# Kernel optimization log

Hardware: AMD Instinct MI355X
Metric: run time of the kernel (lower is better)

The kernel has to match this reference:

```python
import jax, jax.numpy as jnp
import numpy as np

EMBED_DIM = 768
NUM_HEADS = 12
HEAD_DIM = EMBED_DIM // NUM_HEADS
MLP_HIDDEN = int(EMBED_DIM * 4.0)
LN_EPS = 1e-5


def setup_inputs() -> dict:
    key = jax.random.key(0)
    ks = jax.random.split(key, 8)
    C, H = EMBED_DIM, MLP_HIDDEN
    s = 0.02
    return {
        "x": jax.random.normal(ks[0], (2, 2048, C), dtype=jnp.float32),
        "ln1_g": jnp.ones((C,), jnp.float32),
        "ln1_b": jnp.zeros((C,), jnp.float32),
        "qkv_w": jax.random.normal(ks[1], (3 * C, C), jnp.float32) * s,
        "proj_w": jax.random.normal(ks[2], (C, C), jnp.float32) * s,
        "proj_b": jnp.zeros((C,), jnp.float32),
        "ln2_g": jnp.ones((C,), jnp.float32),
        "ln2_b": jnp.zeros((C,), jnp.float32),
        "fc1_w": jax.random.normal(ks[3], (H, C), jnp.float32) * s,
        "fc1_b": jnp.zeros((H,), jnp.float32),
        "fc2_w": jax.random.normal(ks[4], (C, H), jnp.float32) * s,
        "fc2_b": jnp.zeros((C,), jnp.float32),
    }


def _layernorm(x, g, b):
    mu = jnp.mean(x, axis=-1, keepdims=True)
    var = jnp.mean(jnp.square(x - mu), axis=-1, keepdims=True)
    return (x - mu) * jax.lax.rsqrt(var + LN_EPS) * g + b


def reference(x, ln1_g, ln1_b, qkv_w, proj_w, proj_b, ln2_g, ln2_b,
              fc1_w, fc1_b, fc2_w, fc2_b):
    B, N, C = x.shape
    Hh, Dh = NUM_HEADS, HEAD_DIM
    scale = Dh ** -0.5

    # --- attention branch (pre-norm) ---
    h = _layernorm(x, ln1_g, ln1_b)
    qkv = h @ qkv_w.T                                   # [B,N,3C]
    qkv = qkv.reshape(B, N, 3, Hh, Dh)
    q = qkv[:, :, 0].transpose(0, 2, 1, 3)              # [B,H,N,D]
    k = qkv[:, :, 1].transpose(0, 2, 1, 3)
    v = qkv[:, :, 2].transpose(0, 2, 1, 3)
    attn = jnp.einsum('bhnd,bhmd->bhnm', q, k) * scale  # [B,H,N,N]
    attn = jax.nn.softmax(attn, axis=-1)
    o = jnp.einsum('bhnm,bhmd->bhnd', attn, v)          # [B,H,N,D]
    o = o.transpose(0, 2, 1, 3).reshape(B, N, C)
    x = x + o @ proj_w.T + proj_b

    # --- MLP branch (pre-norm), exact GELU like nn.GELU ---
    h = _layernorm(x, ln2_g, ln2_b)
    h = jax.nn.gelu(h @ fc1_w.T + fc1_b, approximate=False)
    x = x + h @ fc2_w.T + fc2_b
    return x
```

## Files before the change

kernel.cpp:

```cpp
#include <hip/hip_runtime.h>
#include <hip/hip_bf16.h>
#include <cstdint>
#include <math.h>


typedef __bf16 bf16_t;
typedef bf16_t bf16x4 __attribute__((ext_vector_type(4)));
typedef bf16_t bf16x8 __attribute__((ext_vector_type(8)));
typedef float floatx4 __attribute__((ext_vector_type(4)));

#define AS1 __attribute__((address_space(1)))
#define AS3 __attribute__((address_space(3)))

__device__ __forceinline__ void async_load16(const void* g, void* l) {
  const AS1 unsigned int* gp =
      reinterpret_cast<const AS1 unsigned int*>(reinterpret_cast<uintptr_t>(g));
  AS3 unsigned int* lp = reinterpret_cast<AS3 unsigned int*>(
      static_cast<unsigned int>(reinterpret_cast<uintptr_t>(l)));
  __builtin_amdgcn_global_load_lds(gp, lp, 16, 0, 0);
}

__device__ __forceinline__ bf16x8 lds_read8(const bf16_t* p) {
  return *reinterpret_cast<const bf16x8*>(p);
}

__global__ __launch_bounds__(256) void cvt_k(const float* __restrict__ in,
                                             bf16_t* __restrict__ out, int n4) {
  const int i = blockIdx.x * 256 + threadIdx.x;
  if (i < n4) {
    const float4 v = reinterpret_cast<const float4*>(in)[i];
    bf16x4 o;
    o[0] = (bf16_t)v.x; o[1] = (bf16_t)v.y; o[2] = (bf16_t)v.z; o[3] = (bf16_t)v.w;
    reinterpret_cast<bf16x4*>(out)[i] = o;
  }
}

__global__ __launch_bounds__(256) void ln_k(const float* __restrict__ x,
                                            const float* __restrict__ g,
                                            const float* __restrict__ b,
                                            bf16_t* __restrict__ out) {
  const int row = blockIdx.x;
  const int tid = threadIdx.x;
  const float* xr = x + (long)row * 768;
  float v[3];
#pragma unroll
  for (int e = 0; e < 3; e++) v[e] = xr[tid + e * 256];
  float s = v[0] + v[1] + v[2];
  float ss = v[0] * v[0] + v[1] * v[1] + v[2] * v[2];
#pragma unroll
  for (int off = 32; off >= 1; off >>= 1) {
    s += __shfl_down(s, off, 64);
    ss += __shfl_down(ss, off, 64);
  }
  __shared__ float red[8];
  __shared__ float stat[2];
  const int wv = tid >> 6;
  if ((tid & 63) == 0) { red[wv] = s; red[4 + wv] = ss; }
  __syncthreads();
  if (tid == 0) {
    float S = red[0] + red[1] + red[2] + red[3];
    float SS = red[4] + red[5] + red[6] + red[7];
    float mu = S * (1.0f / 768.0f);
    float var = SS * (1.0f / 768.0f) - mu * mu;
    stat[0] = mu;
    stat[1] = rsqrtf(var + 1e-5f);
  }
  __syncthreads();
  const float mu = stat[0], rs = stat[1];
#pragma unroll
  for (int e = 0; e < 3; e++) {
    int c = tid + e * 256;
    out[(long)row * 768 + c] = (bf16_t)((v[e] - mu) * rs * g[c] + b[c]);
  }
}

template <int MODE>
__global__ __launch_bounds__(256, 2) void gemm_k(
    const bf16_t* __restrict__ A, const bf16_t* __restrict__ Bt, int lda,
    int ldb, int keff, int Nld, const float* __restrict__ bias,
    bf16_t* __restrict__ out_bf, bf16_t* __restrict__ q_out,
    bf16_t* __restrict__ k_out, bf16_t* __restrict__ vt_out) {
  constexpr int BK = 32;
  __shared__ __align__(16) bf16_t As[2][128 * BK];
  __shared__ __align__(16) bf16_t Bs[2][128 * BK];

  const int tid = threadIdx.x;
  const int w = tid >> 6;
  const int lane = tid & 63;
  const int quad = lane >> 4;
  const int lid = lane & 15;
  const int wr = (w >> 1) * 64;
  const int wc = (w & 1) * 64;
  const int mBase = blockIdx.y * 128;
  const int nBase = blockIdx.x * 128;

  const int ldsRowSub = lane >> 2;
  const int kblk = (lane & 3) ^ (ldsRowSub & 3);
  const int rq0 = (quad ^ (lid & 3)) * 8;
  const int c0 = w * 2, c1 = w * 2 + 1;
  const int rowA0 = c0 * 16 + ldsRowSub, rowA1 = c1 * 16 + ldsRowSub;

  const bf16_t* Ag = A + (long)mBase * lda;
  const bf16_t* Bg = Bt + (long)nBase * ldb;

  floatx4 acc[4][4];
#pragma unroll
  for (int i = 0; i < 4; i++)
#pragma unroll
    for (int j = 0; j < 4; j++) acc[i][j] = (floatx4){0.f, 0.f, 0.f, 0.f};

  async_load16(Ag + (long)rowA0 * lda + kblk * 8, &As[0][c0 * 512]);
  async_load16(Ag + (long)rowA1 * lda + kblk * 8, &As[0][c1 * 512]);
  async_load16(Bg + (long)rowA0 * ldb + kblk * 8, &Bs[0][c0 * 512]);
  async_load16(Bg + (long)rowA1 * ldb + kblk * 8, &Bs[0][c1 * 512]);

  const int iters = keff / BK;
  int cur = 0;
  for (int it = 0; it < iters; it++) {
    __syncthreads();
    if (it + 1 < iters) {
      const int k0 = (it + 1) * BK;
      const int nb = cur ^ 1;
      async_load16(Ag + (long)rowA0 * lda + k0 + kblk * 8, &As[nb][c0 * 512]);
      async_load16(Ag + (long)rowA1 * lda + k0 + kblk * 8, &As[nb][c1 * 512]);
      async_load16(Bg + (long)rowA0 * ldb + k0 + kblk * 8, &Bs[nb][c0 * 512]);
      async_load16(Bg + (long)rowA1 * ldb + k0 + kblk * 8, &Bs[nb][c1 * 512]);
    }

    bf16x8 af[4], bfv[4];
#pragma unroll
    for (int i = 0; i < 4; i++)
      af[i] = lds_read8(&As[cur][(wr + i * 16 + lid) * BK + rq0]);
#pragma unroll
    for (int j = 0; j < 4; j++)
      bfv[j] = lds_read8(&Bs[cur][(wc + j * 16 + lid) * BK + rq0]);
#pragma unroll
    for (int i = 0; i < 4; i++)
#pragma unroll
      for (int j = 0; j < 4; j++)
        acc[i][j] = __builtin_amdgcn_mfma_f32_16x16x32_bf16(af[i], bfv[j],
                                                            acc[i][j], 0, 0, 0);
    cur ^= 1;
  }

#pragma unroll
  for (int i = 0; i < 4; i++) {
    const int mRow = mBase + wr + i * 16 + quad * 4;
#pragma unroll
    for (int j = 0; j < 4; j++) {
      const int n = nBase + wc + j * 16 + lid;
      if constexpr (MODE == 0) {
        const int which = n / 768;
        const int rem = n - which * 768;
        const int head = rem >> 6;
        const int d = rem & 63;
        const int b = mRow >> 11;
        const int t = mRow & 2047;
        const int bh = b * 12 + head;
        if (which == 2) {
          bf16x4 pk;
#pragma unroll
          for (int r = 0; r < 4; r++) pk[r] = (bf16_t)acc[i][j][r];
          const long off = ((long)bh * 64 + d) * 2048 + t;
          *reinterpret_cast<bf16x4*>(&vt_out[off]) = pk;
        } else if (which == 0) {
#pragma unroll
          for (int r = 0; r < 4; r++)
            q_out[((long)bh * 2048 + t + r) * 64 + d] =
                (bf16_t)(acc[i][j][r] * 0.125f);
        } else {
#pragma unroll
          for (int r = 0; r < 4; r++)
            k_out[((long)bh * 2048 + t + r) * 64 + d] = (bf16_t)acc[i][j][r];
        }
      } else {
        const float bv = bias[n];
#pragma unroll
        for (int r = 0; r < 4; r++) {
          float v = acc[i][j][r] + bv;
          float ge = 0.5f * v * (1.0f + erff(v * 0.70710678118654752f));
          out_bf[(long)(mRow + r) * Nld + n] = (bf16_t)ge;
        }
      }
    }
  }
}

template <int MODE>
__global__ __launch_bounds__(256, 2) void gemm64_k(
    const bf16_t* __restrict__ A, const bf16_t* __restrict__ Bt, int lda,
    int ldb, int keff, int Nld, const float* __restrict__ bias,
    const float* __restrict__ resid_f, float* __restrict__ out_f) {
  constexpr int BK = 32;
  __shared__ __align__(16) bf16_t As[2][128 * BK];
  __shared__ __align__(16) bf16_t Bs[2][64 * BK];

  const int tid = threadIdx.x;
  const int w = tid >> 6;
  const int lane = tid & 63;
  const int quad = lane >> 4;
  const int lid = lane & 15;
  const int mBase = blockIdx.y * 128;
  const int nBase = blockIdx.x * 64;

  const int ldsRowSub = lane >> 2;
  const int kblk = (lane & 3) ^ (ldsRowSub & 3);
  const int rq0 = (quad ^ (lid & 3)) * 8;
  const int rowA0 = w * 16 + ldsRowSub;
  const int rowA1 = (w + 4) * 16 + ldsRowSub;

  const bf16_t* Ag = A + (long)mBase * lda;
  const bf16_t* Bg = Bt + (long)nBase * ldb;

  floatx4 acc[2][4];
#pragma unroll
  for (int i = 0; i < 2; i++)
#pragma unroll
    for (int j = 0; j < 4; j++) acc[i][j] = (floatx4){0.f, 0.f, 0.f, 0.f};

  async_load16(Ag + (long)rowA0 * lda + kblk * 8, &As[0][w * 512]);
  async_load16(Ag + (long)rowA1 * lda + kblk * 8, &As[0][(w + 4) * 512]);
  async_load16(Bg + (long)rowA0 * ldb + kblk * 8, &Bs[0][w * 512]);

  const int iters = keff / BK;
  int cur = 0;
  for (int it = 0; it < iters; it++) {
    __syncthreads();
    if (it + 1 < iters) {
      const int k0 = (it + 1) * BK;
      const int nb = cur ^ 1;
      async_load16(Ag + (long)rowA0 * lda + k0 + kblk * 8, &As[nb][w * 512]);
      async_load16(Ag + (long)rowA1 * lda + k0 + kblk * 8, &As[nb][(w + 4) * 512]);
      async_load16(Bg + (long)rowA0 * ldb + k0 + kblk * 8, &Bs[nb][w * 512]);
    }

    bf16x8 af[2], bfv[4];
#pragma unroll
    for (int i = 0; i < 2; i++)
      af[i] = lds_read8(&As[cur][(w * 32 + i * 16 + lid) * BK + rq0]);
#pragma unroll
    for (int j = 0; j < 4; j++)
      bfv[j] = lds_read8(&Bs[cur][(j * 16 + lid) * BK + rq0]);
#pragma unroll
    for (int i = 0; i < 2; i++)
#pragma unroll
      for (int j = 0; j < 4; j++)
        acc[i][j] = __builtin_amdgcn_mfma_f32_16x16x32_bf16(af[i], bfv[j],
                                                            acc[i][j], 0, 0, 0);
    cur ^= 1;
  }

#pragma unroll
  for (int i = 0; i < 2; i++) {
    const int mRow = mBase + w * 32 + i * 16 + quad * 4;
#pragma unroll
    for (int j = 0; j < 4; j++) {
      const int n = nBase + j * 16 + lid;
      if constexpr (MODE == 1) {
        const float bv = bias[n];
#pragma unroll
        for (int r = 0; r < 4; r++) {
          const long off = (long)(mRow + r) * Nld + n;
          out_f[off] = resid_f[off] + acc[i][j][r] + bv;
        }
      } else {
#pragma unroll
        for (int r = 0; r < 4; r++) {
          const long off = (long)(mRow + r) * Nld + n;
          out_f[off] += acc[i][j][r];
        }
      }
    }
  }
}

__global__ __launch_bounds__(256, 2) void flash_k(const bf16_t* __restrict__ q,
                                                  const bf16_t* __restrict__ kk,
                                                  const bf16_t* __restrict__ vt,
                                                  bf16_t* __restrict__ o) {
  constexpr int SK = 64, D = 64, PS = 68;
  __shared__ __align__(16) bf16_t Ks[2][SK * D];
  __shared__ __align__(16) bf16_t Vs[3][D * SK];
  __shared__ __align__(16) bf16_t Ps[4][16 * PS];

  const int tid = threadIdx.x;
  const int w = tid >> 6;
  const int lane = tid & 63;
  const int quad = lane >> 4;
  const int lid = lane & 15;
  const int bh = blockIdx.y;
  const int qBase = blockIdx.x * 64;

  const bf16_t* qg = q + ((long)bh * 2048 + qBase) * D;
  const bf16_t* kg = kk + (long)bh * 2048 * D;
  const bf16_t* vg = vt + (long)bh * D * 2048;

  bf16x8 aq[2];
#pragma unroll
  for (int k2 = 0; k2 < 2; k2++)
    aq[k2] = *reinterpret_cast<const bf16x8*>(qg + (w * 16 + lid) * D +
                                              k2 * 32 + quad * 8);

  const int srow = lane >> 3;
  const int sdb = (lane & 7) ^ srow;
  const int c0 = w * 2, c1 = w * 2 + 1;
  const int rsw = lid & 7;

  async_load16(kg + (long)(c0 * 8 + srow) * D + sdb * 8, &Ks[0][c0 * 512]);
  async_load16(kg + (long)(c1 * 8 + srow) * D + sdb * 8, &Ks[0][c1 * 512]);
  async_load16(vg + (long)(c0 * 8 + srow) * 2048 + sdb * 8, &Vs[0][c0 * 512]);
  async_load16(vg + (long)(c1 * 8 + srow) * 2048 + sdb * 8, &Vs[0][c1 * 512]);

  float lsum = 0.f;
  floatx4 oacc[4];
#pragma unroll
  for (int jo = 0; jo < 4; jo++) oacc[jo] = (floatx4){0.f, 0.f, 0.f, 0.f};

  int kb_cur = 0;
  int vb_cur = 0;
  for (int kci = 0; kci < 32; kci++) {
    __syncthreads();
    if (kci + 1 < 32) {
      const int kc = (kci + 1) * 64;
      const int knb = kb_cur ^ 1;
      const int vnb = (vb_cur == 2) ? 0 : vb_cur + 1;
      async_load16(kg + (long)(kc + c0 * 8 + srow) * D + sdb * 8, &Ks[knb][c0 * 512]);
      async_load16(kg + (long)(kc + c1 * 8 + srow) * D + sdb * 8, &Ks[knb][c1 * 512]);
      async_load16(vg + (long)(c0 * 8 + srow) * 2048 + kc + sdb * 8, &Vs[vnb][c0 * 512]);
      async_load16(vg + (long)(c1 * 8 + srow) * 2048 + kc + sdb * 8, &Vs[vnb][c1 * 512]);
    }

    floatx4 sacc[4];
#pragma unroll
    for (int jm = 0; jm < 4; jm++) sacc[jm] = (floatx4){0.f, 0.f, 0.f, 0.f};
#pragma unroll
    for (int k2 = 0; k2 < 2; k2++) {
#pragma unroll
      for (int jm = 0; jm < 4; jm++) {
        const bf16x8 ak = lds_read8(
            &Ks[kb_cur][(jm * 16 + lid) * D + (((k2 * 4 + quad) ^ rsw) * 8)]);
        sacc[jm] =
            __builtin_amdgcn_mfma_f32_16x16x32_bf16(ak, aq[k2], sacc[jm], 0, 0, 0);
      }
    }

    if (kci > 0) {
      const int vpb = (vb_cur == 0) ? 2 : vb_cur - 1;
#pragma unroll
      for (int k2 = 0; k2 < 2; k2++) {
        const bf16x8 ap = lds_read8(&Ps[w][lid * PS + k2 * 32 + quad * 8]);
#pragma unroll
        for (int jo = 0; jo < 4; jo++) {
          const bf16x8 bv = lds_read8(
              &Vs[vpb][(jo * 16 + lid) * SK + (((k2 * 4 + quad) ^ rsw) * 8)]);
          oacc[jo] =
              __builtin_amdgcn_mfma_f32_16x16x32_bf16(ap, bv, oacc[jo], 0, 0, 0);
        }
      }
    }

#pragma unroll
    for (int jm = 0; jm < 4; jm++) {
      bf16x4 pk;
      float ps = 0.f;
#pragma unroll
      for (int r = 0; r < 4; r++) {
        const float p = exp2f(fmaf(sacc[jm][r], 1.44269504f, -11.5415603f));
        ps += p;
        pk[r] = (bf16_t)p;
      }
      lsum += ps;
      *reinterpret_cast<bf16x4*>(&Ps[w][lid * PS + jm * 16 + quad * 4]) = pk;
    }

    kb_cur ^= 1;
    vb_cur = (vb_cur == 2) ? 0 : vb_cur + 1;
  }

  {
#pragma unroll
    for (int k2 = 0; k2 < 2; k2++) {
      const bf16x8 ap = lds_read8(&Ps[w][lid * PS + k2 * 32 + quad * 8]);
#pragma unroll
      for (int jo = 0; jo < 4; jo++) {
        const bf16x8 bv = lds_read8(
            &Vs[1][(jo * 16 + lid) * SK + (((k2 * 4 + quad) ^ rsw) * 8)]);
        oacc[jo] =
            __builtin_amdgcn_mfma_f32_16x16x32_bf16(ap, bv, oacc[jo], 0, 0, 0);
      }
    }
  }

  lsum += __shfl_xor(lsum, 16, 64);
  lsum += __shfl_xor(lsum, 32, 64);

  const int b = bh / 12;
  const int head = bh - b * 12;
  float lr[4];
#pragma unroll
  for (int r = 0; r < 4; r++) lr[r] = __shfl(lsum, quad * 4 + r, 64);
#pragma unroll
  for (int jo = 0; jo < 4; jo++) {
#pragma unroll
    for (int r = 0; r < 4; r++) {
      const int t = qBase + w * 16 + quad * 4 + r;
      const int col = head * 64 + jo * 16 + lid;
      o[((long)b * 2048 + t) * 768 + col] = (bf16_t)(oacc[jo][r] / lr[r]);
    }
  }
}

extern "C" void kernel_launch(void* const* d_in, const int* in_sizes, int n_in,
                              void* d_out, int out_size, void* d_ws,
                              size_t ws_size, hipStream_t stream) {
  (void)in_sizes; (void)n_in; (void)out_size; (void)ws_size;
  const float* x = (const float*)d_in[0];
  const float* ln1_g = (const float*)d_in[1];
  const float* ln1_b = (const float*)d_in[2];
  const float* qkv_w = (const float*)d_in[3];
  const float* proj_w = (const float*)d_in[4];
  const float* proj_b = (const float*)d_in[5];
  const float* ln2_g = (const float*)d_in[6];
  const float* ln2_b = (const float*)d_in[7];
  const float* fc1_w = (const float*)d_in[8];
  const float* fc1_b = (const float*)d_in[9];
  const float* fc2_w = (const float*)d_in[10];
  const float* fc2_b = (const float*)d_in[11];
  float* out = (float*)d_out;

  char* ws = (char*)d_ws;
  bf16_t* wqkv = (bf16_t*)(ws + 0);
  bf16_t* wproj = (bf16_t*)(ws + 3538944);
  bf16_t* h1 = (bf16_t*)(ws + 4718592);
  bf16_t* ob = (bf16_t*)(ws + 4718592);
  bf16_t* qb = (bf16_t*)(ws + 11010048);
  bf16_t* kb = (bf16_t*)(ws + 17301504);
  bf16_t* vtb = (bf16_t*)(ws + 23592960);
  float* x1 = (float*)(ws + 11010048);
  bf16_t* h2 = (bf16_t*)(ws + 23592960);
  bf16_t* wfc1 = (bf16_t*)(ws + 0);
  bf16_t* wfc2 = (bf16_t*)(ws + 4718592);
  bf16_t* hg = (bf16_t*)(ws + 29884416);

  cvt_k<<<1728, 256, 0, stream>>>(qkv_w, wqkv, 442368);
  cvt_k<<<576, 256, 0, stream>>>(proj_w, wproj, 147456);
  ln_k<<<4096, 256, 0, stream>>>(x, ln1_g, ln1_b, h1);
  gemm_k<0><<<dim3(18, 32), 256, 0, stream>>>(h1, wqkv, 768, 768, 768, 2304,
                                              nullptr, nullptr, qb, kb, vtb);
  flash_k<<<dim3(32, 24), 256, 0, stream>>>(qb, kb, vtb, ob);
  gemm64_k<1><<<dim3(12, 32), 256, 0, stream>>>(ob, wproj, 768, 768, 768, 768,
                                                proj_b, x, x1);
  cvt_k<<<2304, 256, 0, stream>>>(fc1_w, wfc1, 589824);
  cvt_k<<<2304, 256, 0, stream>>>(fc2_w, wfc2, 589824);
  ln_k<<<4096, 256, 0, stream>>>(x1, ln2_g, ln2_b, h2);
  for (int h = 0; h < 2; h++) {
    gemm_k<2><<<dim3(12, 32), 256, 0, stream>>>(h2, wfc1 + (long)h * 1536 * 768,
                                                768, 768, 768, 1536,
                                                fc1_b + h * 1536, hg, nullptr,
                                                nullptr, nullptr);
    if (h == 0)
      gemm64_k<1><<<dim3(12, 32), 256, 0, stream>>>(hg, wfc2 + 0, 1536, 3072,
                                                    1536, 768, fc2_b, x1, out);
    else
      gemm64_k<5><<<dim3(12, 32), 256, 0, stream>>>(hg, wfc2 + 1536, 1536, 3072,
                                                    1536, 768, nullptr, nullptr,
                                                    out);
  }
}
```

Before: 326.4 us.

## Split attention over key halves, merge weight conversions, fuse MLP halves

The flash attention kernel now splits each query tile's keys into two halves across a grid z dimension. Each block uses 512 threads over 128 query rows and double buffers K and V instead of triple buffering V. It writes unnormalized bf16 partial outputs and row sums, which a new combine kernel adds and normalizes. When the workspace is large enough, the four weight conversions are merged into one launch and the MLP runs as a single fc1 GEMM and a single fc2 GEMM instead of two halves. This removes launches and raises flash parallelism, at the cost of extra partial-output traffic and bf16 rounding of the partials.

```diff
diff --git a/kernel.cpp b/kernel.cpp
--- a/kernel.cpp
+++ b/kernel.cpp
@@ -33,6 +33,25 @@
     o[0] = (bf16_t)v.x; o[1] = (bf16_t)v.y; o[2] = (bf16_t)v.z; o[3] = (bf16_t)v.w;
     reinterpret_cast<bf16x4*>(out)[i] = o;
   }
+}
+
+__global__ __launch_bounds__(256) void cvt_all_k(
+    const float* __restrict__ s0, const float* __restrict__ s1,
+    const float* __restrict__ s2, const float* __restrict__ s3,
+    bf16_t* __restrict__ d0, bf16_t* __restrict__ d1, bf16_t* __restrict__ d2,
+    bf16_t* __restrict__ d3) {
+  int i = blockIdx.x * 256 + threadIdx.x;
+  const float* src;
+  bf16_t* dst;
+  if (i < 442368) { src = s0; dst = d0; }
+  else if (i < 589824) { src = s1; dst = d1; i -= 442368; }
+  else if (i < 1179648) { src = s2; dst = d2; i -= 589824; }
+  else if (i < 1769472) { src = s3; dst = d3; i -= 1179648; }
+  else return;
+  const float4 v = reinterpret_cast<const float4*>(src)[i];
+  bf16x4 o;
+  o[0] = (bf16_t)v.x; o[1] = (bf16_t)v.y; o[2] = (bf16_t)v.z; o[3] = (bf16_t)v.w;
+  reinterpret_cast<bf16x4*>(dst)[i] = o;
 }
 
 __global__ __launch_bounds__(256) void ln_k(const float* __restrict__ x,
@@ -274,14 +293,15 @@
   }
 }
 
-__global__ __launch_bounds__(256, 2) void flash_k(const bf16_t* __restrict__ q,
+__global__ __launch_bounds__(512, 1) void flash_k(const bf16_t* __restrict__ q,
                                                   const bf16_t* __restrict__ kk,
                                                   const bf16_t* __restrict__ vt,
-                                                  bf16_t* __restrict__ o) {
+                                                  bf16_t* __restrict__ U,
+                                                  float* __restrict__ lbuf) {
   constexpr int SK = 64, D = 64, PS = 68;
   __shared__ __align__(16) bf16_t Ks[2][SK * D];
-  __shared__ __align__(16) bf16_t Vs[3][D * SK];
-  __shared__ __align__(16) bf16_t Ps[4][16 * PS];
+  __shared__ __align__(16) bf16_t Vs[2][D * SK];
+  __shared__ __align__(16) bf16_t Ps[8][16 * PS];
 
   const int tid = threadIdx.x;
   const int w = tid >> 6;
@@ -289,11 +309,12 @@
   const int quad = lane >> 4;
   const int lid = lane & 15;
   const int bh = blockIdx.y;
-  const int qBase = blockIdx.x * 64;
+  const int half = blockIdx.z;
+  const int qBase = blockIdx.x * 128;
 
   const bf16_t* qg = q + ((long)bh * 2048 + qBase) * D;
-  const bf16_t* kg = kk + (long)bh * 2048 * D;
-  const bf16_t* vg = vt + (long)bh * D * 2048;
+  const bf16_t* kg = kk + ((long)bh * 2048 + half * 1024) * D;
+  const bf16_t* vg = vt + (long)bh * D * 2048 + half * 1024;
 
   bf16x8 aq[2];
 #pragma unroll
@@ -303,31 +324,24 @@
 
   const int srow = lane >> 3;
   const int sdb = (lane & 7) ^ srow;
-  const int c0 = w * 2, c1 = w * 2 + 1;
   const int rsw = lid & 7;
 
-  async_load16(kg + (long)(c0 * 8 + srow) * D + sdb * 8, &Ks[0][c0 * 512]);
-  async_load16(kg + (long)(c1 * 8 + srow) * D + sdb * 8, &Ks[0][c1 * 512]);
-  async_load16(vg + (long)(c0 * 8 + srow) * 2048 + sdb * 8, &Vs[0][c0 * 512]);
-  async_load16(vg + (long)(c1 * 8 + srow) * 2048 + sdb * 8, &Vs[0][c1 * 512]);
+  async_load16(kg + (long)(w * 8 + srow) * D + sdb * 8, &Ks[0][w * 512]);
+  async_load16(vg + (long)(w * 8 + srow) * 2048 + sdb * 8, &Vs[0][w * 512]);
 
   float lsum = 0.f;
   floatx4 oacc[4];
 #pragma unroll
   for (int jo = 0; jo < 4; jo++) oacc[jo] = (floatx4){0.f, 0.f, 0.f, 0.f};
 
-  int kb_cur = 0;
-  int vb_cur = 0;
-  for (int kci = 0; kci < 32; kci++) {
+  int cur = 0;
+  for (int kci = 0; kci < 16; kci++) {
     __syncthreads();
-    if (kci + 1 < 32) {
+    if (kci + 1 < 16) {
       const int kc = (kci + 1) * 64;
-      const int knb = kb_cur ^ 1;
-      const int vnb = (vb_cur == 2) ? 0 : vb_cur + 1;
-      async_load16(kg + (long)(kc + c0 * 8 + srow) * D + sdb * 8, &Ks[knb][c0 * 512]);
-      async_load16(kg + (long)(kc + c1 * 8 + srow) * D + sdb * 8, &Ks[knb][c1 * 512]);
-      async_load16(vg + (long)(c0 * 8 + srow) * 2048 + kc + sdb * 8, &Vs[vnb][c0 * 512]);
-      async_load16(vg + (long)(c1 * 8 + srow) * 2048 + kc + sdb * 8, &Vs[vnb][c1 * 512]);
+      const int nb = cur ^ 1;
+      async_load16(kg + (long)(kc + w * 8 + srow) * D + sdb * 8, &Ks[nb][w * 512]);
+      async_load16(vg + (long)(w * 8 + srow) * 2048 + kc + sdb * 8, &Vs[nb][w * 512]);
     }
 
     floatx4 sacc[4];
@@ -338,24 +352,9 @@
 #pragma unroll
       for (int jm = 0; jm < 4; jm++) {
         const bf16x8 ak = lds_read8(
-            &Ks[kb_cur][(jm * 16 + lid) * D + (((k2 * 4 + quad) ^ rsw) * 8)]);
+            &Ks[cur][(jm * 16 + lid) * D + (((k2 * 4 + quad) ^ rsw) * 8)]);
         sacc[jm] =
             __builtin_amdgcn_mfma_f32_16x16x32_bf16(ak, aq[k2], sacc[jm], 0, 0, 0);
-      }
-    }
-
-    if (kci > 0) {
-      const int vpb = (vb_cur == 0) ? 2 : vb_cur - 1;
-#pragma unroll
-      for (int k2 = 0; k2 < 2; k2++) {
-        const bf16x8 ap = lds_read8(&Ps[w][lid * PS + k2 * 32 + quad * 8]);
-#pragma unroll
-        for (int jo = 0; jo < 4; jo++) {
-          const bf16x8 bv = lds_read8(
-              &Vs[vpb][(jo * 16 + lid) * SK + (((k2 * 4 + quad) ^ rsw) * 8)]);
-          oacc[jo] =
-              __builtin_amdgcn_mfma_f32_16x16x32_bf16(ap, bv, oacc[jo], 0, 0, 0);
-        }
       }
     }
 
@@ -373,47 +372,57 @@
       *reinterpret_cast<bf16x4*>(&Ps[w][lid * PS + jm * 16 + quad * 4]) = pk;
     }
 
-    kb_cur ^= 1;
-    vb_cur = (vb_cur == 2) ? 0 : vb_cur + 1;
-  }
-
-  {
 #pragma unroll
     for (int k2 = 0; k2 < 2; k2++) {
       const bf16x8 ap = lds_read8(&Ps[w][lid * PS + k2 * 32 + quad * 8]);
 #pragma unroll
       for (int jo = 0; jo < 4; jo++) {
         const bf16x8 bv = lds_read8(
-            &Vs[1][(jo * 16 + lid) * SK + (((k2 * 4 + quad) ^ rsw) * 8)]);
+            &Vs[cur][(jo * 16 + lid) * SK + (((k2 * 4 + quad) ^ rsw) * 8)]);
         oacc[jo] =
             __builtin_amdgcn_mfma_f32_16x16x32_bf16(ap, bv, oacc[jo], 0, 0, 0);
       }
     }
+    cur ^= 1;
   }
 
   lsum += __shfl_xor(lsum, 16, 64);
   lsum += __shfl_xor(lsum, 32, 64);
 
+  const long lrow = ((long)half * 24 + bh) * 2048 + qBase + w * 16;
+  if (quad == 0) lbuf[lrow + lid] = lsum;
+
+  bf16_t* Ub = U + (((long)half * 24 + bh) * 2048 + qBase) * D;
+#pragma unroll
+  for (int jo = 0; jo < 4; jo++) {
+#pragma unroll
+    for (int r = 0; r < 4; r++) {
+      const int t = w * 16 + quad * 4 + r;
+      Ub[(long)t * D + jo * 16 + lid] = (bf16_t)oacc[jo][r];
+    }
+  }
+}
+
+__global__ __launch_bounds__(256) void combine_k(const bf16_t* __restrict__ U,
+                                                 const float* __restrict__ lbuf,
+                                                 bf16_t* __restrict__ o) {
+  const int idx = blockIdx.x * 256 + threadIdx.x;
+  const int bh = idx >> 17;
+  const int rem = idx & 131071;
+  const int t = rem >> 6;
+  const int d = rem & 63;
+  const float l0 = lbuf[bh * 2048 + t];
+  const float l1 = lbuf[(24 + bh) * 2048 + t];
+  const float u = (float)U[idx] + (float)U[3145728 + idx];
   const int b = bh / 12;
   const int head = bh - b * 12;
-  float lr[4];
-#pragma unroll
-  for (int r = 0; r < 4; r++) lr[r] = __shfl(lsum, quad * 4 + r, 64);
-#pragma unroll
-  for (int jo = 0; jo < 4; jo++) {
-#pragma unroll
-    for (int r = 0; r < 4; r++) {
-      const int t = qBase + w * 16 + quad * 4 + r;
-      const int col = head * 64 + jo * 16 + lid;
-      o[((long)b * 2048 + t) * 768 + col] = (bf16_t)(oacc[jo][r] / lr[r]);
-    }
-  }
+  o[((long)b * 2048 + t) * 768 + head * 64 + d] = (bf16_t)(u / (l0 + l1));
 }
 
 extern "C" void kernel_launch(void* const* d_in, const int* in_sizes, int n_in,
                               void* d_out, int out_size, void* d_ws,
                               size_t ws_size, hipStream_t stream) {
-  (void)in_sizes; (void)n_in; (void)out_size; (void)ws_size;
+  (void)in_sizes; (void)n_in; (void)out_size;
   const float* x = (const float*)d_in[0];
   const float* ln1_g = (const float*)d_in[1];
   const float* ln1_b = (const float*)d_in[2];
@@ -427,43 +436,80 @@
   const float* fc2_w = (const float*)d_in[10];
   const float* fc2_b = (const float*)d_in[11];
   float* out = (float*)d_out;
-
   char* ws = (char*)d_ws;
-  bf16_t* wqkv = (bf16_t*)(ws + 0);
-  bf16_t* wproj = (bf16_t*)(ws + 3538944);
-  bf16_t* h1 = (bf16_t*)(ws + 4718592);
-  bf16_t* ob = (bf16_t*)(ws + 4718592);
-  bf16_t* qb = (bf16_t*)(ws + 11010048);
-  bf16_t* kb = (bf16_t*)(ws + 17301504);
-  bf16_t* vtb = (bf16_t*)(ws + 23592960);
-  float* x1 = (float*)(ws + 11010048);
-  bf16_t* h2 = (bf16_t*)(ws + 23592960);
-  bf16_t* wfc1 = (bf16_t*)(ws + 0);
-  bf16_t* wfc2 = (bf16_t*)(ws + 4718592);
-  bf16_t* hg = (bf16_t*)(ws + 29884416);
-
-  cvt_k<<<1728, 256, 0, stream>>>(qkv_w, wqkv, 442368);
-  cvt_k<<<576, 256, 0, stream>>>(proj_w, wproj, 147456);
-  ln_k<<<4096, 256, 0, stream>>>(x, ln1_g, ln1_b, h1);
-  gemm_k<0><<<dim3(18, 32), 256, 0, stream>>>(h1, wqkv, 768, 768, 768, 2304,
-                                              nullptr, nullptr, qb, kb, vtb);
-  flash_k<<<dim3(32, 24), 256, 0, stream>>>(qb, kb, vtb, ob);
-  gemm64_k<1><<<dim3(12, 32), 256, 0, stream>>>(ob, wproj, 768, 768, 768, 768,
-                                                proj_b, x, x1);
-  cvt_k<<<2304, 256, 0, stream>>>(fc1_w, wfc1, 589824);
-  cvt_k<<<2304, 256, 0, stream>>>(fc2_w, wfc2, 589824);
-  ln_k<<<4096, 256, 0, stream>>>(x1, ln2_g, ln2_b, h2);
-  for (int h = 0; h < 2; h++) {
-    gemm_k<2><<<dim3(12, 32), 256, 0, stream>>>(h2, wfc1 + (long)h * 1536 * 768,
-                                                768, 768, 768, 1536,
-                                                fc1_b + h * 1536, hg, nullptr,
-                                                nullptr, nullptr);
-    if (h == 0)
-      gemm64_k<1><<<dim3(12, 32), 256, 0, stream>>>(hg, wfc2 + 0, 1536, 3072,
-                                                    1536, 768, fc2_b, x1, out);
-    else
-      gemm64_k<5><<<dim3(12, 32), 256, 0, stream>>>(hg, wfc2 + 1536, 1536, 3072,
-                                                    1536, 768, nullptr, nullptr,
-                                                    out);
-  }
-}
+
+  const bool big = ws_size >= (size_t)64487424;
+
+  if (big) {
+    bf16_t* wqkv = (bf16_t*)(ws + 0);
+    bf16_t* wproj = (bf16_t*)(ws + 3538944);
+    bf16_t* wfc1 = (bf16_t*)(ws + 4718592);
+    bf16_t* wfc2 = (bf16_t*)(ws + 9437184);
+    bf16_t* h1 = (bf16_t*)(ws + 14155776);
+    bf16_t* ob = h1;
+    bf16_t* qb = (bf16_t*)(ws + 20447232);
+    bf16_t* kb = (bf16_t*)(ws + 26738688);
+    bf16_t* vtb = (bf16_t*)(ws + 33030144);
+    bf16_t* Ubuf = (bf16_t*)(ws + 39321600);
+    float* lbuf = (float*)(ws + 51904512);
+    float* x1 = (float*)(ws + 20447232);
+    bf16_t* h2 = (bf16_t*)(ws + 33030144);
+    bf16_t* hg = (bf16_t*)(ws + 39321600);
+
+    cvt_all_k<<<6912, 256, 0, stream>>>(qkv_w, proj_w, fc1_w, fc2_w, wqkv,
+                                        wproj, wfc1, wfc2);
+    ln_k<<<4096, 256, 0, stream>>>(x, ln1_g, ln1_b, h1);
+    gemm_k<0><<<dim3(18, 32), 256, 0, stream>>>(h1, wqkv, 768, 768, 768, 2304,
+                                                nullptr, nullptr, qb, kb, vtb);
+    flash_k<<<dim3(16, 24, 2), 512, 0, stream>>>(qb, kb, vtb, Ubuf, lbuf);
+    combine_k<<<12288, 256, 0, stream>>>(Ubuf, lbuf, ob);
+    gemm64_k<1><<<dim3(12, 32), 256, 0, stream>>>(ob, wproj, 768, 768, 768, 768,
+                                                  proj_b, x, x1);
+    ln_k<<<4096, 256, 0, stream>>>(x1, ln2_g, ln2_b, h2);
+    gemm_k<2><<<dim3(24, 32), 256, 0, stream>>>(h2, wfc1, 768, 768, 768, 3072,
+                                                fc1_b, hg, nullptr, nullptr,
+                                                nullptr);
+    gemm64_k<1><<<dim3(12, 32), 256, 0, stream>>>(hg, wfc2, 3072, 3072, 3072,
+                                                  768, fc2_b, x1, out);
+  } else {
+    bf16_t* wqkv = (bf16_t*)(ws + 0);
+    bf16_t* wproj = (bf16_t*)(ws + 3538944);
+    bf16_t* h1 = (bf16_t*)(ws + 4718592);
+    bf16_t* ob = h1;
+    bf16_t* qb = (bf16_t*)(ws + 11010048);
+    bf16_t* kb = (bf16_t*)(ws + 17301504);
+    bf16_t* vtb = (bf16_t*)(ws + 23592960);
+    float* x1 = (float*)(ws + 11010048);
+    bf16_t* h2 = (bf16_t*)(ws + 23592960);
+    bf16_t* wfc1 = (bf16_t*)(ws + 0);
+    bf16_t* wfc2 = (bf16_t*)(ws + 4718592);
+    bf16_t* hg = (bf16_t*)(ws + 29884416);
+    bf16_t* Ubuf = (bf16_t*)(ws + 29884416);
+    float* lbuf = (float*)(ws + 42467328);
+
+    cvt_k<<<1728, 256, 0, stream>>>(qkv_w, wqkv, 442368);
+    cvt_k<<<576, 256, 0, stream>>>(proj_w, wproj, 147456);
+    ln_k<<<4096, 256, 0, stream>>>(x, ln1_g, ln1_b, h1);
+    gemm_k<0><<<dim3(18, 32), 256, 0, stream>>>(h1, wqkv, 768, 768, 768, 2304,
+                                                nullptr, nullptr, qb, kb, vtb);
+    flash_k<<<dim3(16, 24, 2), 512, 0, stream>>>(qb, kb, vtb, Ubuf, lbuf);
+    combine_k<<<12288, 256, 0, stream>>>(Ubuf, lbuf, ob);
+    gemm64_k<1><<<dim3(12, 32), 256, 0, stream>>>(ob, wproj, 768, 768, 768, 768,
+                                                  proj_b, x, x1);
+    cvt_k<<<2304, 256, 0, stream>>>(fc1_w, wfc1, 589824);
+    cvt_k<<<2304, 256, 0, stream>>>(fc2_w, wfc2, 589824);
+    ln_k<<<4096, 256, 0, stream>>>(x1, ln2_g, ln2_b, h2);
+    for (int h = 0; h < 2; h++) {
+      gemm_k<2><<<dim3(12, 32), 256, 0, stream>>>(
+          h2, wfc1 + (long)h * 1536 * 768, 768, 768, 768, 1536,
+          fc1_b + h * 1536, hg, nullptr, nullptr, nullptr);
+      if (h == 0)
+        gemm64_k<1><<<dim3(12, 32), 256, 0, stream>>>(hg, wfc2 + 0, 1536, 3072,
+                                                      1536, 768, fc2_b, x1, out);
+      else
+        gemm64_k<5><<<dim3(12, 32), 256, 0, stream>>>(hg, wfc2 + 1536, 1536,
+                                                      3072, 1536, 768, nullptr,
+                                                      nullptr, out);
+    }
+  }
+}
```

Result: faster. 293.6 us (-10.0%).
